# Kernel optimization log

Hardware: AMD Instinct MI355X
Metric: run time of the kernel (lower is better)

Reference implementation:

```python
import math
import jax, jax.numpy as jnp
import numpy as np

B, N = 8, 2048
IN_DIM = COND_DIM = ATTN_DIM = OUT_DIM = 128
NUM_HEADS = 4
DH = ATTN_DIM // NUM_HEADS  # 32


def setup_inputs() -> dict:
    key = jax.random.key(0)
    ks = jax.random.split(key, 10)
    s_in = 1.0 / math.sqrt(IN_DIM)
    s_cd = 1.0 / math.sqrt(COND_DIM)
    return {
        "x": jax.random.normal(ks[0], (B, N, IN_DIM), jnp.float32),
        "cond": jax.random.normal(ks[1], (B, N, COND_DIM), jnp.float32),
        "flags": jnp.ones((B, N, 1), jnp.float32),
        "attention_mask": jax.random.normal(ks[2], (B, N, N), jnp.float32),
        # Linear params (stored [in, out]; torch Linear is x @ W.T + b)
        "Wq": jax.random.uniform(ks[3], (IN_DIM, ATTN_DIM), jnp.float32, -s_in, s_in),
        "bq": jax.random.uniform(ks[4], (ATTN_DIM,), jnp.float32, -s_in, s_in),
        "Wk": jax.random.uniform(ks[5], (COND_DIM, ATTN_DIM), jnp.float32, -s_cd, s_cd),
        "bk": jax.random.uniform(ks[6], (ATTN_DIM,), jnp.float32, -s_cd, s_cd),
        "Wv": jax.random.uniform(ks[7], (COND_DIM, OUT_DIM), jnp.float32, -s_cd, s_cd),
        "bv": jax.random.uniform(ks[8], (OUT_DIM,), jnp.float32, -s_cd, s_cd),
    }


def reference(x, cond, flags, attention_mask, Wq, bq, Wk, bk, Wv, bv):
    # flags is accepted but unused, matching the original forward.
    b, n, _ = x.shape
    Q = (x @ Wq + bq).reshape(b, n, NUM_HEADS, DH)     # channel-split heads
    K = (cond @ Wk + bk).reshape(b, n, NUM_HEADS, DH)
    V = cond @ Wv + bv                                 # [B, N, OUT_DIM]
    # per-head scores, scaled by sqrt(out_dim) as in the original
    S = jnp.einsum("bnhd,bmhd->hbnm", Q, K) / math.sqrt(OUT_DIM)
    A = jnp.tanh(attention_mask[None] + S)             # tanh activation, not softmax
    A = A.mean(axis=0)                                 # head-mean -> [B, N, N]
    return jnp.einsum("bnm,bmd->bnd", A, V)
```

## Files before the change

### kernel.cpp

```cpp
#include <hip/hip_runtime.h>
#include <hip/hip_bf16.h>

typedef __attribute__((ext_vector_type(4))) float f32x4;
typedef __attribute__((ext_vector_type(8))) short bf16x8;

#define MFMA16(A, B, C) __builtin_amdgcn_mfma_f32_16x16x32_bf16(A, B, C, 0, 0, 0)

#define C2 2.8853900817779268f
#define QS (2.8853900817779268f / 11.313708498984761f)

__device__ __forceinline__ unsigned cvtpk_bf16(float lo, float hi) {
    unsigned r;
    asm("v_cvt_pk_bf16_f32 %0, %1, %2" : "=v"(r) : "v"(lo), "v"(hi));
    return r;
}

__device__ __forceinline__ bf16x8 pack8(float4 a, float4 b) {
    union { unsigned u[4]; bf16x8 v; } u;
    u.u[0] = cvtpk_bf16(a.x, a.y);
    u.u[1] = cvtpk_bf16(a.z, a.w);
    u.u[2] = cvtpk_bf16(b.x, b.y);
    u.u[3] = cvtpk_bf16(b.z, b.w);
    return u.v;
}

__device__ __forceinline__ void gload_lds16(const void* g, void* l) {
    __builtin_amdgcn_global_load_lds(
        (const __attribute__((address_space(1))) unsigned int*)g,
        (__attribute__((address_space(3))) unsigned int*)l, 16, 0, 0);
}

__global__ void prep_weights(const float* __restrict__ Wq, const float* __restrict__ bq,
                             const float* __restrict__ Wk, const float* __restrict__ bk,
                             const float* __restrict__ Wv, const float* __restrict__ bv,
                             __hip_bfloat16* __restrict__ Wqt, __hip_bfloat16* __restrict__ Wkt,
                             __hip_bfloat16* __restrict__ Wvt, float* __restrict__ bias) {
    int i = blockIdx.x * 256 + threadIdx.x;
    int k = i >> 7, o = i & 127;
    Wqt[o * 128 + k] = __float2bfloat16(Wq[i] * QS);
    Wkt[o * 128 + k] = __float2bfloat16(Wk[i]);
    Wvt[o * 128 + k] = __float2bfloat16(Wv[i] * 0.25f);
    if (i < 128) {
        bias[i]       = bq[i] * QS;
        bias[128 + i] = bk[i];
        bias[256 + i] = bv[i] * 0.25f;
    }
}

__global__ __launch_bounds__(256) void proj_qkv(
        const float* __restrict__ x, const float* __restrict__ cond,
        const __hip_bfloat16* __restrict__ Wqt, const __hip_bfloat16* __restrict__ Wkt,
        const __hip_bfloat16* __restrict__ Wvt, const float* __restrict__ bias,
        __hip_bfloat16* __restrict__ Qo, __hip_bfloat16* __restrict__ Ko,
        __hip_bfloat16* __restrict__ Vt) {
    const int lane = threadIdx.x & 63, wv = threadIdx.x >> 6;
    const int l15 = lane & 15, g = lane >> 4;
    const int row0 = blockIdx.x * 64 + wv * 16;

    f32x4 qa[8], ka[8], va[8];
#pragma unroll
    for (int ot = 0; ot < 8; ++ot) {
        float b0 = bias[16 * ot + l15];
        float b1 = bias[128 + 16 * ot + l15];
        float b2 = bias[256 + 16 * ot + l15];
        qa[ot] = (f32x4){b0, b0, b0, b0};
        ka[ot] = (f32x4){b1, b1, b1, b1};
        va[ot] = (f32x4){b2, b2, b2, b2};
    }

    const float* xp = x    + (size_t)(row0 + l15) * 128 + 8 * g;
    const float* cp = cond + (size_t)(row0 + l15) * 128 + 8 * g;
#pragma unroll
    for (int kk = 0; kk < 4; ++kk) {
        float4 x0 = *(const float4*)(xp + 32 * kk);
        float4 x1 = *(const float4*)(xp + 32 * kk + 4);
        float4 c0 = *(const float4*)(cp + 32 * kk);
        float4 c1 = *(const float4*)(cp + 32 * kk + 4);
        bf16x8 xa = pack8(x0, x1);
        bf16x8 ca = pack8(c0, c1);
#pragma unroll
        for (int ot = 0; ot < 8; ++ot) {
            const int wo = (16 * ot + l15) * 128 + 32 * kk + 8 * g;
            qa[ot] = MFMA16(xa, *(const bf16x8*)(Wqt + wo), qa[ot]);
            ka[ot] = MFMA16(ca, *(const bf16x8*)(Wkt + wo), ka[ot]);
            va[ot] = MFMA16(ca, *(const bf16x8*)(Wvt + wo), va[ot]);
        }
    }

#pragma unroll
    for (int ot = 0; ot < 8; ++ot)
#pragma unroll
        for (int r = 0; r < 4; ++r) {
            size_t idx = (size_t)(row0 + 4 * g + r) * 128 + 16 * ot + l15;
            Qo[idx] = __float2bfloat16(qa[ot][r]);
            Ko[idx] = __float2bfloat16(ka[ot][r]);
        }
    const int bb = row0 >> 11, nn = (row0 & 2047) + 4 * g;
#pragma unroll
    for (int ot = 0; ot < 8; ++ot) {
        uint2 pr;
        pr.x = cvtpk_bf16(va[ot][0], va[ot][1]);
        pr.y = cvtpk_bf16(va[ot][2], va[ot][3]);
        *(uint2*)((unsigned short*)Vt + ((size_t)bb * 128 + 16 * ot + l15) * 2048 + nn) = pr;
    }
}

__global__ __launch_bounds__(512) void attn_main(
        const __hip_bfloat16* __restrict__ Q, const __hip_bfloat16* __restrict__ K,
        const __hip_bfloat16* __restrict__ Vt, const float* __restrict__ mask,
        float* __restrict__ out) {
    __shared__ __align__(16) char Kl[2][8192];
    __shared__ __align__(16) char Vl[3][8192];
    __shared__ __align__(16) char Al[2][4608];

    const int lane = threadIdx.x & 63, w = threadIdx.x >> 6;
    const int l15 = lane & 15, g = lane >> 4;
    const int qw = w & 3, mw = w >> 2, dw = mw;
    const int qt = blockIdx.x & 31;
    const int mh = (blockIdx.x >> 5) & 1;
    const int b  = blockIdx.x >> 6;
    const int n0 = qt * 64;
    const int mh0 = mh * 1024;

    const __hip_bfloat16* Qb = Q + ((size_t)b * 2048 + n0 + qw * 16) * 128;
    const char* Kg = (const char*)(K + (size_t)b * 2048 * 128);
    const char* Vg = (const char*)(Vt + (size_t)b * 128 * 2048);
    const float* mrow = mask + ((size_t)b * 2048 + n0 + qw * 16 + l15) * 2048
                        + mh0 + mw * 16 + 4 * g;

    bf16x8 qf[4];
#pragma unroll
    for (int h = 0; h < 4; ++h)
        qf[h] = *(const bf16x8*)(Qb + l15 * 128 + 32 * h + 8 * g);

    f32x4 oacc[4];
#pragma unroll
    for (int dtl = 0; dtl < 4; ++dtl) oacc[dtl] = (f32x4){0.f, 0.f, 0.f, 0.f};
    const f32x4 zero = (f32x4){0.f, 0.f, 0.f, 0.f};

    auto STAGE = [&](int m0g, int kb, int vb) {
        const int o = w * 1024 + lane * 16;
        const int kr = o >> 8, kc = o & 255;
        gload_lds16(Kg + (size_t)(m0g + kr) * 256 + (kc ^ ((kr & 15) << 4)),
                    &Kl[kb][w * 1024]);
        const int vr = o >> 6, vc = o & 63;
        gload_lds16(Vg + (size_t)vr * 4096 + (size_t)m0g * 2 + (vc ^ ((vr & 3) << 4)),
                    &Vl[vb][w * 1024]);
    };

    STAGE(mh0, 0, 0);
    f32x4 mkc = *(const f32x4*)(mrow);
    asm volatile("s_waitcnt vmcnt(0)" ::: "memory");
    __builtin_amdgcn_s_barrier();

    int vb_st = 1;
    int vb_pv = 2;

#pragma unroll 2
    for (int c = 0; c < 32; ++c) {
        const int abi = c & 1;
        f32x4 mkn;
        if (c < 31) {
            STAGE(mh0 + (c + 1) * 32, abi ^ 1, vb_st);
            mkn = *(const f32x4*)(mrow + (c + 1) * 32);
        }

        {
            const int mr = mw * 16 + l15;
            const char* kb = &Kl[abi][mr * 256];
            const int sw = l15 << 4;
            f32x4 s0 = MFMA16(*(const bf16x8*)(kb + ((g * 16) ^ sw)),       qf[0], zero);
            f32x4 s1 = MFMA16(*(const bf16x8*)(kb + ((64 + g * 16) ^ sw)),  qf[1], zero);
            f32x4 s2 = MFMA16(*(const bf16x8*)(kb + ((128 + g * 16) ^ sw)), qf[2], zero);
            f32x4 s3 = MFMA16(*(const bf16x8*)(kb + ((192 + g * 16) ^ sw)), qf[3], zero);
            float acd[4];
#pragma unroll
            for (int r = 0; r < 4; ++r) {
                float m2 = mkc[r] * C2;
                float e0 = __builtin_amdgcn_exp2f(m2 + s0[r]);
                float e1 = __builtin_amdgcn_exp2f(m2 + s1[r]);
                float e2 = __builtin_amdgcn_exp2f(m2 + s2[r]);
                float e3 = __builtin_amdgcn_exp2f(m2 + s3[r]);
                float rs = __builtin_amdgcn_rcpf(1.f + e0) + __builtin_amdgcn_rcpf(1.f + e1)
                         + __builtin_amdgcn_rcpf(1.f + e2) + __builtin_amdgcn_rcpf(1.f + e3);
                acd[r] = 4.f - 2.f * rs;
            }
            uint2 pk;
            pk.x = cvtpk_bf16(acd[0], acd[1]);
            pk.y = cvtpk_bf16(acd[2], acd[3]);
            *(uint2*)(&Al[abi][(qw * 16 + l15) * 72 + (mw * 16 + 4 * g) * 2]) = pk;
        }

        if (c > 0) {
            bf16x8 af = *(const bf16x8*)(&Al[abi ^ 1][(qw * 16 + l15) * 72 + g * 16]);
#pragma unroll
            for (int dtl = 0; dtl < 4; ++dtl) {
                const int dr = dw * 64 + dtl * 16 + l15;
                bf16x8 vf = *(const bf16x8*)(
                    &Vl[vb_pv][dr * 64 + ((g * 16) ^ ((dr & 3) << 4))]);
                oacc[dtl] = MFMA16(af, vf, oacc[dtl]);
            }
        }

        asm volatile("s_waitcnt vmcnt(0) lgkmcnt(0)" ::: "memory");
        __builtin_amdgcn_s_barrier();

        mkc = mkn;
        vb_st = (vb_st == 2) ? 0 : vb_st + 1;
        vb_pv = (vb_pv == 2) ? 0 : vb_pv + 1;
    }

    {
        bf16x8 af = *(const bf16x8*)(&Al[1][(qw * 16 + l15) * 72 + g * 16]);
#pragma unroll
        for (int dtl = 0; dtl < 4; ++dtl) {
            const int dr = dw * 64 + dtl * 16 + l15;
            bf16x8 vf = *(const bf16x8*)(
                &Vl[vb_pv][dr * 64 + ((g * 16) ^ ((dr & 3) << 4))]);
            oacc[dtl] = MFMA16(af, vf, oacc[dtl]);
        }
    }

    float* ob = out + ((size_t)b * 2048 + n0 + qw * 16) * 128 + dw * 64;
#pragma unroll
    for (int dtl = 0; dtl < 4; ++dtl)
#pragma unroll
        for (int r = 0; r < 4; ++r)
            unsafeAtomicAdd(&ob[(size_t)(4 * g + r) * 128 + dtl * 16 + l15], oacc[dtl][r]);
}

extern "C" void kernel_launch(void* const* d_in, const int* in_sizes, int n_in,
                              void* d_out, int out_size, void* d_ws, size_t ws_size,
                              hipStream_t stream) {
    const float* x    = (const float*)d_in[0];
    const float* cond = (const float*)d_in[1];
    const float* mask = (const float*)d_in[3];
    const float* Wq = (const float*)d_in[4];
    const float* bq = (const float*)d_in[5];
    const float* Wk = (const float*)d_in[6];
    const float* bk = (const float*)d_in[7];
    const float* Wv = (const float*)d_in[8];
    const float* bv = (const float*)d_in[9];
    float* out = (float*)d_out;

    char* ws = (char*)d_ws;
    __hip_bfloat16* Qo  = (__hip_bfloat16*)(ws);
    __hip_bfloat16* Ko  = (__hip_bfloat16*)(ws + (4  << 20));
    __hip_bfloat16* Vt  = (__hip_bfloat16*)(ws + (8  << 20));
    __hip_bfloat16* Wqt = (__hip_bfloat16*)(ws + (12 << 20));
    __hip_bfloat16* Wkt = (__hip_bfloat16*)(ws + (12 << 20) + 32768);
    __hip_bfloat16* Wvt = (__hip_bfloat16*)(ws + (12 << 20) + 65536);
    float*          bias = (float*)(ws + (12 << 20) + 98304);

    hipMemsetAsync(d_out, 0, (size_t)out_size * sizeof(float), stream);

    prep_weights<<<64, 256, 0, stream>>>(Wq, bq, Wk, bk, Wv, bv, Wqt, Wkt, Wvt, bias);
    proj_qkv<<<256, 256, 0, stream>>>(x, cond, Wqt, Wkt, Wvt, bias, Qo, Ko, Vt);
    attn_main<<<512, 512, 0, stream>>>(Qo, Ko, Vt, mask, out);
}
```

Measured before the change: 88.87 us.

## Prefetch K tiles and mask two iterations ahead with triple-buffered K

Splits the staging lambda so K tiles and mask values are fetched two chunks ahead while V stays one chunk ahead. K gets a third LDS buffer and the per-iteration barrier now waits with partial vmcnt instead of draining all outstanding loads. The goal is to hide global/mask load latency behind the score and PV MFMAs. The A tile row stride also changes from 72 to 80 bytes, shifting LDS bank mapping. Costs are more LDS (lower occupancy headroom) and fragile hand-counted vmcnt values.

Result: slower. 91.07 us (+2.5%).

```diff
diff --git a/kernel.cpp b/kernel.cpp
--- a/kernel.cpp
+++ b/kernel.cpp
@@ -109,9 +109,9 @@
         const __hip_bfloat16* __restrict__ Q, const __hip_bfloat16* __restrict__ K,
         const __hip_bfloat16* __restrict__ Vt, const float* __restrict__ mask,
         float* __restrict__ out) {
-    __shared__ __align__(16) char Kl[2][8192];
+    __shared__ __align__(16) char Kl[3][8192];
     __shared__ __align__(16) char Vl[3][8192];
-    __shared__ __align__(16) char Al[2][4608];
+    __shared__ __align__(16) char Al[2][5120];
 
     const int lane = threadIdx.x & 63, w = threadIdx.x >> 6;
     const int l15 = lane & 15, g = lane >> 4;
@@ -138,36 +138,44 @@
     for (int dtl = 0; dtl < 4; ++dtl) oacc[dtl] = (f32x4){0.f, 0.f, 0.f, 0.f};
     const f32x4 zero = (f32x4){0.f, 0.f, 0.f, 0.f};
 
-    auto STAGE = [&](int m0g, int kb, int vb) {
+    auto STAGE_K = [&](int m0g, int kb) {
         const int o = w * 1024 + lane * 16;
         const int kr = o >> 8, kc = o & 255;
         gload_lds16(Kg + (size_t)(m0g + kr) * 256 + (kc ^ ((kr & 15) << 4)),
                     &Kl[kb][w * 1024]);
+    };
+    auto STAGE_V = [&](int m0g, int vb) {
+        const int o = w * 1024 + lane * 16;
         const int vr = o >> 6, vc = o & 63;
         gload_lds16(Vg + (size_t)vr * 4096 + (size_t)m0g * 2 + (vc ^ ((vr & 3) << 4)),
                     &Vl[vb][w * 1024]);
     };
 
-    STAGE(mh0, 0, 0);
+    STAGE_K(mh0, 0);
+    STAGE_V(mh0, 0);
     f32x4 mkc = *(const f32x4*)(mrow);
-    asm volatile("s_waitcnt vmcnt(0)" ::: "memory");
+    asm volatile("" ::: "memory");
+    STAGE_K(mh0 + 32, 1);
+    f32x4 mkn = *(const f32x4*)(mrow + 32);
+    asm volatile("s_waitcnt vmcnt(2)" ::: "memory");
     __builtin_amdgcn_s_barrier();
 
-    int vb_st = 1;
-    int vb_pv = 2;
+    int kb_st = 2, kb_rd = 0;
+    int vb_st = 1, vb_pv = 2;
 
 #pragma unroll 2
     for (int c = 0; c < 32; ++c) {
         const int abi = c & 1;
-        f32x4 mkn;
-        if (c < 31) {
-            STAGE(mh0 + (c + 1) * 32, abi ^ 1, vb_st);
-            mkn = *(const f32x4*)(mrow + (c + 1) * 32);
-        }
+        f32x4 mk2;
+        if (c < 30) {
+            STAGE_K(mh0 + (c + 2) * 32, kb_st);
+            mk2 = *(const f32x4*)(mrow + (c + 2) * 32);
+        }
+        if (c < 31) STAGE_V(mh0 + (c + 1) * 32, vb_st);
 
         {
             const int mr = mw * 16 + l15;
-            const char* kb = &Kl[abi][mr * 256];
+            const char* kb = &Kl[kb_rd][mr * 256];
             const int sw = l15 << 4;
             f32x4 s0 = MFMA16(*(const bf16x8*)(kb + ((g * 16) ^ sw)),       qf[0], zero);
             f32x4 s1 = MFMA16(*(const bf16x8*)(kb + ((64 + g * 16) ^ sw)),  qf[1], zero);
@@ -188,11 +196,11 @@
             uint2 pk;
             pk.x = cvtpk_bf16(acd[0], acd[1]);
             pk.y = cvtpk_bf16(acd[2], acd[3]);
-            *(uint2*)(&Al[abi][(qw * 16 + l15) * 72 + (mw * 16 + 4 * g) * 2]) = pk;
+            *(uint2*)(&Al[abi][(qw * 16 + l15) * 80 + (mw * 16 + 4 * g) * 2]) = pk;
         }
 
         if (c > 0) {
-            bf16x8 af = *(const bf16x8*)(&Al[abi ^ 1][(qw * 16 + l15) * 72 + g * 16]);
+            bf16x8 af = *(const bf16x8*)(&Al[abi ^ 1][(qw * 16 + l15) * 80 + g * 16]);
 #pragma unroll
             for (int dtl = 0; dtl < 4; ++dtl) {
                 const int dr = dw * 64 + dtl * 16 + l15;
@@ -202,16 +210,21 @@
             }
         }
 
-        asm volatile("s_waitcnt vmcnt(0) lgkmcnt(0)" ::: "memory");
+        if (c < 30)       asm volatile("s_waitcnt vmcnt(3)" ::: "memory");
+        else if (c == 30) asm volatile("s_waitcnt vmcnt(2)" ::: "memory");
+        else              asm volatile("s_waitcnt vmcnt(0)" ::: "memory");
+        asm volatile("s_waitcnt lgkmcnt(0)" ::: "memory");
         __builtin_amdgcn_s_barrier();
 
-        mkc = mkn;
+        mkc = mkn; mkn = mk2;
+        kb_st = (kb_st == 2) ? 0 : kb_st + 1;
+        kb_rd = (kb_rd == 2) ? 0 : kb_rd + 1;
         vb_st = (vb_st == 2) ? 0 : vb_st + 1;
         vb_pv = (vb_pv == 2) ? 0 : vb_pv + 1;
     }
 
     {
-        bf16x8 af = *(const bf16x8*)(&Al[1][(qw * 16 + l15) * 72 + g * 16]);
+        bf16x8 af = *(const bf16x8*)(&Al[1][(qw * 16 + l15) * 80 + g * 16]);
 #pragma unroll
         for (int dtl = 0; dtl < 4; ++dtl) {
             const int dr = dw * 64 + dtl * 16 + l15;
```
